# Optimization experiments

Hardware: AMD Instinct MI355X
Metric: run time of the kernel (lower is better)

Reference implementation:

```python
import jax, jax.numpy as jnp
import numpy as np
from jax import lax

K = 2048  # nb_subsampled_points


def setup_inputs() -> dict:
    key = jax.random.key(0)
    k1, k2 = jax.random.split(key)
    B, N, D = 32, 131072, 3
    x = jax.random.normal(k1, (B, N, D), dtype=jnp.float32)
    start_idx = jax.random.randint(k2, (B,), 0, N, dtype=jnp.int64)
    return {"x": x, "start_idx": start_idx}


def reference(x, start_idx):
    """Iterative farthest point sampling.

    x: [B, N, D] point cloud, start_idx: [B] initial centroid indices.
    Returns [B, K] int indices of the sampled centroids.
    """
    B, N, D = x.shape

    def step(carry, _):
        min_d, idx = carry                                   # [B,N], [B]
        centroid = jnp.take_along_axis(x, idx[:, None, None], axis=1)  # [B,1,D]
        dist = jnp.sqrt(jnp.sum((x - centroid) ** 2, axis=2))          # [B,N]
        min_d = jnp.minimum(min_d, dist)
        next_idx = jnp.argmax(min_d, axis=1)                 # farthest point
        return (min_d, next_idx), idx

    init = (jnp.full((B, N), jnp.inf, dtype=x.dtype), start_idx.astype(jnp.int32))
    _, idxs = lax.scan(step, init, None, length=K)           # [K, B]
    return idxs.T                                            # [B, K]
```

## Files before the change

### kernel.cpp

```cpp
#include <hip/hip_runtime.h>

#define NB 32
#define NPTS 131072
#define KSAMP 2048
#define TPB 512


#define RPT16(X) X(0)X(1)X(2)X(3)X(4)X(5)X(6)X(7)X(8)X(9)X(10)X(11)X(12) \
  X(13)X(14)X(15)
#define RPT32(X) RPT16(X) X(16)X(17)X(18)X(19)X(20)X(21)X(22)X(23)X(24) \
  X(25)X(26)X(27)X(28)X(29)X(30)X(31)

#define DECLP(J) float px##J, py##J, pz##J, md2##J;
#define INITP(J) { const int n = base + (J) * TPB;          \
    px##J = xb[3*n]; py##J = xb[3*n+1]; pz##J = xb[3*n+2];  \
    md2##J = __builtin_inff(); }
#define SCANP(J) {                                              \
    const float dx = px##J - cx;                                \
    const float dy = py##J - cy;                                \
    const float dz = pz##J - cz;                                \
    const float d2 = fmaf(dz, dz, fmaf(dx, dx, dy * dy));       \
    const float m  = fminf(md2##J, d2);                         \
    md2##J = m;                                                 \
    if (m > bestv) { bestv = m; bestn = base + (J) * TPB; }     \
  }

__device__ __forceinline__ int read_start(const int* start, int b) {
  bool is64 = true;
  #pragma unroll 1
  for (int i = 1; i < 32; i += 2) {
    if (start[i] != 0) { is64 = false; break; }
  }
  return is64 ? start[2 * b] : start[b];
}

#define NPART16 16
#define PART_PTS16 (NPTS / NPART16)

__global__ __launch_bounds__(TPB, 4) void fps_kernel16(
    const float* __restrict__ x, const int* __restrict__ start,
    int* __restrict__ out, unsigned long long* __restrict__ slot)
{
  #pragma clang fp contract(off)
  const int blk  = blockIdx.x;
  const int xcd  = blk & 7;
  const int j    = blk >> 3;
  const int b    = xcd * 4 + (j & 3);
  const int part = j >> 2;
  const int tid  = threadIdx.x;
  const int lane = tid & 63;
  const int wave = tid >> 6;

  const float* xb = x + (size_t)b * (NPTS * 3);
  int cur = read_start(start, b);
  const int base = part * PART_PTS16 + tid;

  RPT16(DECLP)
  RPT16(INITP)

  __shared__ unsigned long long wred[TPB / 64];
  __shared__ int snext;

  if (part == 0 && tid == 0) out[b * KSAMP] = cur;

  float cx = xb[3 * (size_t)cur + 0];
  float cy = xb[3 * (size_t)cur + 1];
  float cz = xb[3 * (size_t)cur + 2];

  unsigned long long* const srow0 = slot + (size_t)b * 2 * NPART16;

  for (int k = 0; k < KSAMP - 1; ++k) {
    float bestv = -1.0f;
    int   bestn = 0;
    RPT16(SCANP)

    const float sdw = sqrtf(bestv);

    unsigned long long key =
        ((unsigned long long)__float_as_uint(sdw) << 32) |
        (unsigned int)(NPTS - 1 - bestn);

    #pragma unroll
    for (int off = 32; off >= 1; off >>= 1) {
      unsigned long long o = __shfl_xor(key, off, 64);
      if (o > key) key = o;
    }
    if (lane == 0) wred[wave] = key;
    __syncthreads();

    if (wave == 0) {
      unsigned long long v = wred[lane & 7];
      #pragma unroll
      for (int off = 4; off >= 1; off >>= 1) {
        unsigned long long o = __shfl_xor(v, off, 64);
        if (o > v) v = o;
      }

      const unsigned tag = (unsigned)(k + 1);
      unsigned long long* const row = srow0 + (unsigned)(k & 1) * NPART16;
      if (lane == 0)
        __hip_atomic_store(&row[part], v | ((unsigned long long)tag << 17),
                           __ATOMIC_RELAXED, __HIP_MEMORY_SCOPE_AGENT);

      unsigned long long g;
      do {
        g = __hip_atomic_load(&row[lane & (NPART16 - 1)], __ATOMIC_RELAXED,
                              __HIP_MEMORY_SCOPE_AGENT);
      } while (__ballot(((unsigned)(g >> 17) & 0x7FFFu) == tag) != ~0ull);

      #pragma unroll
      for (int off = 8; off >= 1; off >>= 1) {
        unsigned long long o = __shfl_xor(g, off, 64);
        if (o > g) g = o;
      }
      const int nidx = NPTS - 1 - (int)(g & 0x1FFFFu);
      if (lane == 0) {
        snext = nidx;
        if (part == 0) out[b * KSAMP + k + 1] = nidx;
      }
    }
    __syncthreads();

    const int nidx = snext;
    cx = xb[3 * (size_t)nidx + 0];
    cy = xb[3 * (size_t)nidx + 1];
    cz = xb[3 * (size_t)nidx + 2];
  }
}

#define NPART32 8
#define PART_PTS32 (NPTS / NPART32)

__global__ __launch_bounds__(TPB)
__attribute__((amdgpu_waves_per_eu(2, 2)))
void fps_kernel32(
    const float* __restrict__ x, const int* __restrict__ start,
    int* __restrict__ out, unsigned long long* __restrict__ slot)
{
  #pragma clang fp contract(off)
  const int blk  = blockIdx.x;
  const int xcd  = blk & 7;
  const int j    = blk >> 3;
  const int b    = xcd * 4 + (j & 3);
  const int part = j >> 2;
  const int tid  = threadIdx.x;
  const int lane = tid & 63;
  const int wave = tid >> 6;

  const float* xb = x + (size_t)b * (NPTS * 3);
  int cur = read_start(start, b);
  const int base = part * PART_PTS32 + tid;

  RPT32(DECLP)
  RPT32(INITP)

  __shared__ unsigned long long wred[TPB / 64];
  __shared__ int snext;

  if (part == 0 && tid == 0) out[b * KSAMP] = cur;

  float cx = xb[3 * (size_t)cur + 0];
  float cy = xb[3 * (size_t)cur + 1];
  float cz = xb[3 * (size_t)cur + 2];

  unsigned long long* const srow0 = slot + (size_t)b * 2 * NPART32;

  for (int k = 0; k < KSAMP - 1; ++k) {
    float bestv = -1.0f;
    int   bestn = 0;
    RPT32(SCANP)

    const float sdw = sqrtf(bestv);

    unsigned long long key =
        ((unsigned long long)__float_as_uint(sdw) << 32) |
        (unsigned int)(NPTS - 1 - bestn);

    #pragma unroll
    for (int off = 32; off >= 1; off >>= 1) {
      unsigned long long o = __shfl_xor(key, off, 64);
      if (o > key) key = o;
    }
    if (lane == 0) wred[wave] = key;
    __syncthreads();

    if (wave == 0) {
      unsigned long long v = wred[lane & 7];
      #pragma unroll
      for (int off = 4; off >= 1; off >>= 1) {
        unsigned long long o = __shfl_xor(v, off, 64);
        if (o > v) v = o;
      }

      const unsigned tag = (unsigned)(k + 1);
      unsigned long long* const row = srow0 + (unsigned)(k & 1) * NPART32;
      if (lane == 0)
        __hip_atomic_store(&row[part], v | ((unsigned long long)tag << 17),
                           __ATOMIC_RELAXED, __HIP_MEMORY_SCOPE_AGENT);

      unsigned long long g;
      do {
        g = __hip_atomic_load(&row[lane & (NPART32 - 1)], __ATOMIC_RELAXED,
                              __HIP_MEMORY_SCOPE_AGENT);
      } while (__ballot(((unsigned)(g >> 17) & 0x7FFFu) == tag) != ~0ull);

      #pragma unroll
      for (int off = 4; off >= 1; off >>= 1) {
        unsigned long long o = __shfl_xor(g, off, 64);
        if (o > g) g = o;
      }
      const int nidx = NPTS - 1 - (int)(g & 0x1FFFFu);
      if (lane == 0) {
        snext = nidx;
        if (part == 0) out[b * KSAMP + k + 1] = nidx;
      }
    }
    __syncthreads();

    const int nidx = snext;
    cx = xb[3 * (size_t)nidx + 0];
    cy = xb[3 * (size_t)nidx + 1];
    cz = xb[3 * (size_t)nidx + 2];
  }
}

extern "C" void kernel_launch(void* const* d_in, const int* in_sizes, int n_in,
                              void* d_out, int out_size, void* d_ws, size_t ws_size,
                              hipStream_t stream) {
  const float* x     = (const float*)d_in[0];
  const int*   start = (const int*)d_in[1];
  int*         out   = (int*)d_out;
  unsigned long long* slot = (unsigned long long*)d_ws;

  void* args[] = {(void*)&x, (void*)&start, (void*)&out, (void*)&slot};

  int occ = 0;
  (void)hipOccupancyMaxActiveBlocksPerMultiprocessor(
      &occ, (const void*)fps_kernel16, TPB, 0);
  if (occ >= 2) {
    hipLaunchCooperativeKernel((void*)fps_kernel16, dim3(NB * NPART16),
                               dim3(TPB), args, 0, stream);
  } else {
    hipLaunchCooperativeKernel((void*)fps_kernel32, dim3(NB * NPART32),
                               dim3(TPB), args, 0, stream);
  }
}
```

Measured before the change: 4.644 ms.

## Repack points to SoA workspace and stream coordinates per iteration

```diff
diff --git a/kernel.cpp b/kernel.cpp
--- a/kernel.cpp
+++ b/kernel.cpp
@@ -3,27 +3,18 @@
 #define NB 32
 #define NPTS 131072
 #define KSAMP 2048
+#define NPART 8
 #define TPB 512
-
-
-#define RPT16(X) X(0)X(1)X(2)X(3)X(4)X(5)X(6)X(7)X(8)X(9)X(10)X(11)X(12) \
-  X(13)X(14)X(15)
-#define RPT32(X) RPT16(X) X(16)X(17)X(18)X(19)X(20)X(21)X(22)X(23)X(24) \
-  X(25)X(26)X(27)X(28)X(29)X(30)X(31)
-
-#define DECLP(J) float px##J, py##J, pz##J, md2##J;
-#define INITP(J) { const int n = base + (J) * TPB;          \
-    px##J = xb[3*n]; py##J = xb[3*n+1]; pz##J = xb[3*n+2];  \
-    md2##J = __builtin_inff(); }
-#define SCANP(J) {                                              \
-    const float dx = px##J - cx;                                \
-    const float dy = py##J - cy;                                \
-    const float dz = pz##J - cz;                                \
-    const float d2 = fmaf(dz, dz, fmaf(dx, dx, dy * dy));       \
-    const float m  = fminf(md2##J, d2);                         \
-    md2##J = m;                                                 \
-    if (m > bestv) { bestv = m; bestn = base + (J) * TPB; }     \
-  }
+#define NPT 32
+#define PART_PTS (NPTS / NPART)
+#define BATCH_F (NPTS * 3)
+#define SOA_BYTES ((size_t)NB * BATCH_F * 4)
+
+
+#define GRP8(X) X(0)X(1)X(2)X(3)X(4)X(5)X(6)X(7)
+#define RPT32(X) X(0)X(1)X(2)X(3)X(4)X(5)X(6)X(7)X(8)X(9)X(10)X(11)X(12) \
+  X(13)X(14)X(15)X(16)X(17)X(18)X(19)X(20)X(21)X(22)X(23)X(24)X(25)X(26) \
+  X(27)X(28)X(29)X(30)X(31)
 
 __device__ __forceinline__ int read_start(const int* start, int b) {
   bool is64 = true;
@@ -34,10 +25,145 @@
   return is64 ? start[2 * b] : start[b];
 }
 
-#define NPART16 16
-#define PART_PTS16 (NPTS / NPART16)
-
-__global__ __launch_bounds__(TPB, 4) void fps_kernel16(
+__global__ __launch_bounds__(256) void repack_kernel(
+    const float* __restrict__ x, float* __restrict__ W)
+{
+  const int blk = blockIdx.x;
+  const int b   = blk >> 6;
+  const int c   = blk & 63;
+  const int t   = threadIdx.x;
+  const float* xb = x + (size_t)b * BATCH_F;
+  float* X = W + (size_t)b * BATCH_F;
+  float* Y = X + NPTS;
+  float* Z = Y + NPTS;
+  #pragma unroll
+  for (int i = 0; i < 8; ++i) {
+    const int n = c * 2048 + i * 256 + t;
+    X[n] = xb[3 * n + 0];
+    Y[n] = xb[3 * n + 1];
+    Z[n] = xb[3 * n + 2];
+  }
+}
+
+__global__ __launch_bounds__(TPB, 2) void fps_soa(
+    const float* __restrict__ W, const int* __restrict__ start,
+    int* __restrict__ out, unsigned long long* __restrict__ slot)
+{
+  #pragma clang fp contract(off)
+  const int blk  = blockIdx.x;
+  const int xcd  = blk & 7;
+  const int j    = blk >> 3;
+  const int b    = xcd * 4 + (j & 3);
+  const int part = j >> 2;
+  const int tid  = threadIdx.x;
+  const int lane = tid & 63;
+  const int wave = tid >> 6;
+
+  const float* Xb = W + (size_t)b * BATCH_F;
+  const float* Yb = Xb + NPTS;
+  const float* Zb = Yb + NPTS;
+
+  int cur = read_start(start, b);
+  const int S = part * PART_PTS;
+
+  const float4* Xt = (const float4*)(Xb + S) + wave * 512 + lane;
+  const float4* Yt = (const float4*)(Yb + S) + wave * 512 + lane;
+  const float4* Zt = (const float4*)(Zb + S) + wave * 512 + lane;
+  const int nbase = S + wave * 2048 + lane * 4;
+
+  #define DECLG(G) float md2_##G##_0 = __builtin_inff(),  \
+      md2_##G##_1 = __builtin_inff(),                     \
+      md2_##G##_2 = __builtin_inff(),                     \
+      md2_##G##_3 = __builtin_inff();
+  GRP8(DECLG)
+
+  __shared__ unsigned long long wred[TPB / 64];
+  __shared__ int snext;
+
+  if (part == 0 && tid == 0) out[b * KSAMP] = cur;
+
+  float cx = Xb[cur], cy = Yb[cur], cz = Zb[cur];
+
+  unsigned long long* const srow0 = slot + (size_t)b * 2 * NPART;
+
+  for (int k = 0; k < KSAMP - 1; ++k) {
+    float bestv = -1.0f;
+    int   bestn = 0;
+    #define SC(G,I,XX,YY,ZZ) {                                  \
+      const float dx = (XX) - cx;                               \
+      const float dy = (YY) - cy;                               \
+      const float dz = (ZZ) - cz;                               \
+      const float d2 = fmaf(dz, dz, fmaf(dx, dx, dy * dy));     \
+      const float m  = fminf(md2_##G##_##I, d2);                \
+      md2_##G##_##I = m;                                        \
+      if (m > bestv) { bestv = m; bestn = nbase + (G)*256 + (I); } }
+    #define SCANG(G) {                                          \
+      const float4 xv = Xt[(G) * 64];                           \
+      const float4 yv = Yt[(G) * 64];                           \
+      const float4 zv = Zt[(G) * 64];                           \
+      SC(G,0,xv.x,yv.x,zv.x)                                    \
+      SC(G,1,xv.y,yv.y,zv.y)                                    \
+      SC(G,2,xv.z,yv.z,zv.z)                                    \
+      SC(G,3,xv.w,yv.w,zv.w) }
+    GRP8(SCANG)
+
+    const float sdw = sqrtf(bestv);
+
+    unsigned long long key =
+        ((unsigned long long)__float_as_uint(sdw) << 32) |
+        (unsigned int)(NPTS - 1 - bestn);
+
+    #pragma unroll
+    for (int off = 32; off >= 1; off >>= 1) {
+      unsigned long long o = __shfl_xor(key, off, 64);
+      if (o > key) key = o;
+    }
+    if (lane == 0) wred[wave] = key;
+    __syncthreads();
+
+    if (wave == 0) {
+      unsigned long long v = wred[lane & 7];
+      #pragma unroll
+      for (int off = 4; off >= 1; off >>= 1) {
+        unsigned long long o = __shfl_xor(v, off, 64);
+        if (o > v) v = o;
+      }
+
+      const unsigned tag = (unsigned)(k + 1);
+      unsigned long long* const row = srow0 + (unsigned)(k & 1) * NPART;
+      if (lane == 0)
+        __hip_atomic_store(&row[part], v | ((unsigned long long)tag << 17),
+                           __ATOMIC_RELAXED, __HIP_MEMORY_SCOPE_AGENT);
+
+      unsigned long long g;
+      do {
+        g = __hip_atomic_load(&row[lane & (NPART - 1)], __ATOMIC_RELAXED,
+                              __HIP_MEMORY_SCOPE_AGENT);
+      } while (__ballot(((unsigned)(g >> 17) & 0x7FFFu) == tag) != ~0ull);
+
+      #pragma unroll
+      for (int off = 4; off >= 1; off >>= 1) {
+        unsigned long long o = __shfl_xor(g, off, 64);
+        if (o > g) g = o;
+      }
+      const int nidx = NPTS - 1 - (int)(g & 0x1FFFFu);
+      if (lane == 0) {
+        snext = nidx;
+        if (part == 0) out[b * KSAMP + k + 1] = nidx;
+      }
+    }
+    __syncthreads();
+
+    const int nidx = snext;
+    cx = Xb[nidx];
+    cy = Yb[nidx];
+    cz = Zb[nidx];
+  }
+}
+
+__global__ __launch_bounds__(TPB)
+__attribute__((amdgpu_waves_per_eu(2, 2)))
+void fps_aos(
     const float* __restrict__ x, const int* __restrict__ start,
     int* __restrict__ out, unsigned long long* __restrict__ slot)
 {
@@ -51,12 +177,16 @@
   const int lane = tid & 63;
   const int wave = tid >> 6;
 
-  const float* xb = x + (size_t)b * (NPTS * 3);
+  const float* xb = x + (size_t)b * BATCH_F;
   int cur = read_start(start, b);
-  const int base = part * PART_PTS16 + tid;
-
-  RPT16(DECLP)
-  RPT16(INITP)
+  const int base = part * PART_PTS + tid;
+
+  #define DECLP(J) float px##J, py##J, pz##J, md2##J;
+  RPT32(DECLP)
+  #define INITP(J) { const int n = base + (J) * TPB;          \
+      px##J = xb[3*n]; py##J = xb[3*n+1]; pz##J = xb[3*n+2];  \
+      md2##J = __builtin_inff(); }
+  RPT32(INITP)
 
   __shared__ unsigned long long wred[TPB / 64];
   __shared__ int snext;
@@ -67,12 +197,21 @@
   float cy = xb[3 * (size_t)cur + 1];
   float cz = xb[3 * (size_t)cur + 2];
 
-  unsigned long long* const srow0 = slot + (size_t)b * 2 * NPART16;
+  unsigned long long* const srow0 = slot + (size_t)b * 2 * NPART;
 
   for (int k = 0; k < KSAMP - 1; ++k) {
     float bestv = -1.0f;
     int   bestn = 0;
-    RPT16(SCANP)
+    #define SCANP(J) {                                              \
+      const float dx = px##J - cx;                                  \
+      const float dy = py##J - cy;                                  \
+      const float dz = pz##J - cz;                                  \
+      const float d2 = fmaf(dz, dz, fmaf(dx, dx, dy * dy));         \
+      const float m  = fminf(md2##J, d2);                           \
+      md2##J = m;                                                   \
+      if (m > bestv) { bestv = m; bestn = base + (J) * TPB; }       \
+    }
+    RPT32(SCANP)
 
     const float sdw = sqrtf(bestv);
 
@@ -95,112 +234,15 @@
         unsigned long long o = __shfl_xor(v, off, 64);
         if (o > v) v = o;
       }
-
       const unsigned tag = (unsigned)(k + 1);
-      unsigned long long* const row = srow0 + (unsigned)(k & 1) * NPART16;
+      unsigned long long* const row = srow0 + (unsigned)(k & 1) * NPART;
       if (lane == 0)
         __hip_atomic_store(&row[part], v | ((unsigned long long)tag << 17),
                            __ATOMIC_RELAXED, __HIP_MEMORY_SCOPE_AGENT);
 
       unsigned long long g;
       do {
-        g = __hip_atomic_load(&row[lane & (NPART16 - 1)], __ATOMIC_RELAXED,
-                              __HIP_MEMORY_SCOPE_AGENT);
-      } while (__ballot(((unsigned)(g >> 17) & 0x7FFFu) == tag) != ~0ull);
-
-      #pragma unroll
-      for (int off = 8; off >= 1; off >>= 1) {
-        unsigned long long o = __shfl_xor(g, off, 64);
-        if (o > g) g = o;
-      }
-      const int nidx = NPTS - 1 - (int)(g & 0x1FFFFu);
-      if (lane == 0) {
-        snext = nidx;
-        if (part == 0) out[b * KSAMP + k + 1] = nidx;
-      }
-    }
-    __syncthreads();
-
-    const int nidx = snext;
-    cx = xb[3 * (size_t)nidx + 0];
-    cy = xb[3 * (size_t)nidx + 1];
-    cz = xb[3 * (size_t)nidx + 2];
-  }
-}
-
-#define NPART32 8
-#define PART_PTS32 (NPTS / NPART32)
-
-__global__ __launch_bounds__(TPB)
-__attribute__((amdgpu_waves_per_eu(2, 2)))
-void fps_kernel32(
-    const float* __restrict__ x, const int* __restrict__ start,
-    int* __restrict__ out, unsigned long long* __restrict__ slot)
-{
-  #pragma clang fp contract(off)
-  const int blk  = blockIdx.x;
-  const int xcd  = blk & 7;
-  const int j    = blk >> 3;
-  const int b    = xcd * 4 + (j & 3);
-  const int part = j >> 2;
-  const int tid  = threadIdx.x;
-  const int lane = tid & 63;
-  const int wave = tid >> 6;
-
-  const float* xb = x + (size_t)b * (NPTS * 3);
-  int cur = read_start(start, b);
-  const int base = part * PART_PTS32 + tid;
-
-  RPT32(DECLP)
-  RPT32(INITP)
-
-  __shared__ unsigned long long wred[TPB / 64];
-  __shared__ int snext;
-
-  if (part == 0 && tid == 0) out[b * KSAMP] = cur;
-
-  float cx = xb[3 * (size_t)cur + 0];
-  float cy = xb[3 * (size_t)cur + 1];
-  float cz = xb[3 * (size_t)cur + 2];
-
-  unsigned long long* const srow0 = slot + (size_t)b * 2 * NPART32;
-
-  for (int k = 0; k < KSAMP - 1; ++k) {
-    float bestv = -1.0f;
-    int   bestn = 0;
-    RPT32(SCANP)
-
-    const float sdw = sqrtf(bestv);
-
-    unsigned long long key =
-        ((unsigned long long)__float_as_uint(sdw) << 32) |
-        (unsigned int)(NPTS - 1 - bestn);
-
-    #pragma unroll
-    for (int off = 32; off >= 1; off >>= 1) {
-      unsigned long long o = __shfl_xor(key, off, 64);
-      if (o > key) key = o;
-    }
-    if (lane == 0) wred[wave] = key;
-    __syncthreads();
-
-    if (wave == 0) {
-      unsigned long long v = wred[lane & 7];
-      #pragma unroll
-      for (int off = 4; off >= 1; off >>= 1) {
-        unsigned long long o = __shfl_xor(v, off, 64);
-        if (o > v) v = o;
-      }
-
-      const unsigned tag = (unsigned)(k + 1);
-      unsigned long long* const row = srow0 + (unsigned)(k & 1) * NPART32;
-      if (lane == 0)
-        __hip_atomic_store(&row[part], v | ((unsigned long long)tag << 17),
-                           __ATOMIC_RELAXED, __HIP_MEMORY_SCOPE_AGENT);
-
-      unsigned long long g;
-      do {
-        g = __hip_atomic_load(&row[lane & (NPART32 - 1)], __ATOMIC_RELAXED,
+        g = __hip_atomic_load(&row[lane & (NPART - 1)], __ATOMIC_RELAXED,
                               __HIP_MEMORY_SCOPE_AGENT);
       } while (__ballot(((unsigned)(g >> 17) & 0x7FFFu) == tag) != ~0ull);
 
@@ -230,18 +272,18 @@
   const float* x     = (const float*)d_in[0];
   const int*   start = (const int*)d_in[1];
   int*         out   = (int*)d_out;
-  unsigned long long* slot = (unsigned long long*)d_ws;
-
-  void* args[] = {(void*)&x, (void*)&start, (void*)&out, (void*)&slot};
-
-  int occ = 0;
-  (void)hipOccupancyMaxActiveBlocksPerMultiprocessor(
-      &occ, (const void*)fps_kernel16, TPB, 0);
-  if (occ >= 2) {
-    hipLaunchCooperativeKernel((void*)fps_kernel16, dim3(NB * NPART16),
-                               dim3(TPB), args, 0, stream);
+
+  if (ws_size >= SOA_BYTES + 4096) {
+    float* W = (float*)d_ws;
+    unsigned long long* slot = (unsigned long long*)((char*)d_ws + SOA_BYTES);
+    repack_kernel<<<dim3(NB * 64), dim3(256), 0, stream>>>(x, W);
+    void* args[] = {(void*)&W, (void*)&start, (void*)&out, (void*)&slot};
+    hipLaunchCooperativeKernel((void*)fps_soa, dim3(NB * NPART), dim3(TPB),
+                               args, 0, stream);
   } else {
-    hipLaunchCooperativeKernel((void*)fps_kernel32, dim3(NB * NPART32),
-                               dim3(TPB), args, 0, stream);
-  }
-}
+    unsigned long long* slot = (unsigned long long*)d_ws;
+    void* args[] = {(void*)&x, (void*)&start, (void*)&out, (void*)&slot};
+    hipLaunchCooperativeKernel((void*)fps_aos, dim3(NB * NPART), dim3(TPB),
+                               args, 0, stream);
+  }
+}
```

Result: slower. 4.879 ms (+5.1%).
